# Kernel optimization log

Hardware: AMD Instinct MI355X
Metric: run time of the kernel (lower is better)

Reference implementation:

```python
import jax, jax.numpy as jnp
import numpy as np

B = 1024      # number of states
NP = 32       # SVGD particles per state
AD = 20       # act_dim
OD = 64       # obs_dim
H = 256       # critic hidden width
STEPS = 5     # num_svgd_steps
LR = 0.1      # svgd_lr (adaptive_lr disabled)
SP0 = 1.0     # svgd_sigma_p0
ALIM = 1.0    # act_limit


def _q(obs, X, w1, b1, w2, b2, w3, b3):
    h = jnp.concatenate([obs, X], axis=-1)
    h = jax.nn.relu(h @ w1 + b1)
    h = jax.nn.relu(h @ w2 + b2)
    return jnp.squeeze(h @ w3 + b3, -1)


def _rbf(X):
    # X: [B, NP, AD] -> K [B,NP,NP], diff [B,NP,NP,AD], gamma [B,1,1], K_grad [B,NP,NP,AD]
    diff = X[:, :, None, :] - X[:, None, :, :]
    dist_sq = jnp.sum(diff * diff, axis=-1)
    # adaptive bandwidth via median heuristic (adaptive_sig=True)
    med = jnp.median(dist_sq.reshape(dist_sq.shape[0], -1), axis=-1)
    sig_sq = med / (2.0 * jnp.log(NP + 1.0))
    gamma = (1.0 / (2.0 * sig_sq + 1e-8))[:, None, None]
    K = jnp.exp(-gamma * dist_sq)
    K_grad = -2.0 * gamma[..., None] * diff * K[..., None]  # d/dx_i K(x_i, x_j)
    return K, diff, gamma, K_grad


def setup_inputs():
    key = jax.random.key(0)
    ks = jax.random.split(key, 16)
    N = B * NP

    def lin(k, fi, fo):
        return (jax.random.normal(k, (fi, fo), jnp.float32) / np.sqrt(fi)).astype(jnp.float32)

    return {
        "obs": jax.random.normal(ks[0], (N, OD), jnp.float32),
        "a0": jax.random.normal(ks[1], (N, AD), jnp.float32) * np.sqrt(SP0),
        "q1_w1": lin(ks[2], OD + AD, H), "q1_b1": jnp.zeros((H,), jnp.float32),
        "q1_w2": lin(ks[3], H, H),       "q1_b2": jnp.zeros((H,), jnp.float32),
        "q1_w3": lin(ks[4], H, 1),       "q1_b3": jnp.zeros((1,), jnp.float32),
        "q2_w1": lin(ks[5], OD + AD, H), "q2_b1": jnp.zeros((H,), jnp.float32),
        "q2_w2": lin(ks[6], H, H),       "q2_b2": jnp.zeros((H,), jnp.float32),
        "q2_w3": lin(ks[7], H, 1),       "q2_b3": jnp.zeros((1,), jnp.float32),
    }


def reference(obs, a0, q1_w1, q1_b1, q1_w2, q1_b2, q1_w3, q1_b3,
              q2_w1, q2_b1, q2_w2, q2_b2, q2_w3, q2_b3):
    eye = jnp.eye(NP, dtype=a0.dtype)

    def q_min_sum(Xf):
        q1 = _q(obs, Xf, q1_w1, q1_b1, q1_w2, q1_b2, q1_w3, q1_b3)
        q2 = _q(obs, Xf, q2_w1, q2_b1, q2_w2, q2_b2, q2_w3, q2_b3)
        return jnp.sum(jnp.minimum(q1, q2))

    score_fn = jax.grad(q_min_sum)  # autograd score function

    def step(carry, _):
        a, logp = carry
        score = score_fn(a).reshape(-1, NP, AD)                 # [B,NP,AD]
        X = a.reshape(-1, NP, AD)
        K, diff, gamma, Kg = _rbf(X)
        phi = (jnp.einsum('bij,bjd->bid', K, score) + Kg.sum(axis=1)) / NP
        # log-prob correction terms (with_logprob=True)
        term1 = jnp.mean(jnp.sum(Kg * score[:, None, :, :], axis=-1), axis=2)     # [B,NP]
        inner = jnp.sum(jnp.transpose(Kg, (0, 2, 1, 3)) * diff, axis=-1) \
                - AD * (K - eye)
        term2 = -2.0 * gamma[:, :, 0] * jnp.mean(inner, axis=1)                   # [B,NP]
        logp = logp - LR * (term1 + term2)
        a = a + LR * phi.reshape(a.shape)                        # svgd_optim
        return (a, logp), None

    logp0 = jnp.zeros((B, NP), a0.dtype)
    (a, logp_svgd), _ = jax.lax.scan(step, (a0, logp0), None, length=STEPS)

    a_sq = ALIM * jnp.tanh(a)                                    # [B*NP, AD]
    logp_normal = (-AD * 0.5 * jnp.log(2.0 * jnp.pi * SP0)
                   - 0.5 / SP0 * jnp.sum(a0 * a0, axis=-1)).reshape(-1, NP)
    logp_tanh = -jnp.sum(2.0 * (jnp.log(2.0) - a - jax.nn.softplus(-2.0 * a)),
                         axis=-1).reshape(-1, NP)
    logp_a = jnp.mean(logp_normal + logp_svgd + logp_tanh, axis=-1)  # [B]
    return a_sq, logp_a
```

## Files before the change

### kernel.cpp

```cpp
#include <hip/hip_runtime.h>
#include <math.h>

#define NPART 32
#define ADIM  20
#define ODIM  64
#define HID   256
#define NSTEPS 5
#define LRC   0.1f
#define NBLK  512
#define LOG33 3.4965075614664802f
#define A0LD  104

typedef short bf8 __attribute__((ext_vector_type(8)));
typedef short s4b __attribute__((ext_vector_type(4)));
typedef float f4  __attribute__((ext_vector_type(4)));
typedef unsigned u4 __attribute__((ext_vector_type(4)));

#define OW1T(n) ((n)*24576)
#define OW2T(n) (49152 + (n)*65536)
#define OW2C(n) (180224 + (n)*65536)
#define OW1X(n) (311296 + (n)*8192)
#define WS_ELEMS 327680

__device__ __forceinline__ short f2bf(float x) {
    unsigned u = __float_as_uint(x);
    u += 0x7FFFu + ((u >> 16) & 1u);
    return (short)(u >> 16);
}
__device__ __forceinline__ short f2bfT(float x) {
    return (short)(__float_as_uint(x) >> 16);
}
__device__ __forceinline__ float bf2f(short s) {
    return __uint_as_float(((unsigned)(unsigned short)s) << 16);
}

#define MFMA(a,b,c) __builtin_amdgcn_mfma_f32_16x16x32_bf16((a),(b),(c),0,0,0)

__global__ void prep_weights(const float* __restrict__ w1a, const float* __restrict__ w2a,
                             const float* __restrict__ w3a, const float* __restrict__ w1b,
                             const float* __restrict__ w2b, const float* __restrict__ w3b,
                             unsigned short* __restrict__ ws)
{
    int idx = blockIdx.x * 256 + threadIdx.x;
    if (idx >= WS_ELEMS) return;
    float val;
    if (idx < 49152) {
        int net = idx / 24576, rem = idx % 24576;
        int n = rem / 96, k = rem % 96;
        const float* w1 = net ? w1b : w1a;
        val = (k < 84) ? w1[k*256 + n] : 0.f;
    } else if (idx < 180224) {
        int t2 = idx - 49152; int net = t2 / 65536, rem = t2 % 65536;
        int n = rem / 256, k = rem % 256;
        const float* w2 = net ? w2b : w2a;
        val = w2[k*256 + n];
    } else if (idx < 311296) {
        int t2 = idx - 180224; int net = t2 / 65536, rem = t2 % 65536;
        const float* w2 = net ? w2b : w2a;
        const float* w3 = net ? w3b : w3a;
        val = w2[rem] * w3[rem % 256];
    } else {
        int t2 = idx - 311296; int net = t2 / 8192, rem = t2 % 8192;
        int d = rem / 256, n = rem % 256;
        const float* w1 = net ? w1b : w1a;
        val = (d < 20) ? w1[(64 + d)*256 + n] : 0.f;
    }
    ws[idx] = (unsigned short)f2bf(val);
}

__global__ void __launch_bounds__(512, 4)
svgd_main(const float* __restrict__ obs,  const float* __restrict__ a0g,
          const float* __restrict__ b1a,  const float* __restrict__ b2a, const float* __restrict__ b3a,
          const float* __restrict__ b1b,  const float* __restrict__ b2b, const float* __restrict__ b3b,
          const float* __restrict__ w3af, const float* __restrict__ w3bf,
          const unsigned short* __restrict__ ws, float* __restrict__ out)
{
    __shared__ __align__(16) short A0s[64*A0LD];
    __shared__ __align__(16) short hbuf[64*264];
    __shared__ unsigned maskS[2][2][64][8];
    __shared__ float Xm[64*20];
    __shared__ float scoreS[64*21];
    __shared__ float qpart[2][8][64];
    __shared__ int   winsS[64];
    __shared__ float logps[64];
    __shared__ unsigned short lutI[496], lutJ[496];
    __shared__ float med2[4];
    __shared__ float qvS[64];
    __shared__ float normsS[64], rowKS[64];
    __shared__ __align__(16) float diagS[64];

    float* d2sF = (float*)hbuf;
    float* GSF  = ((float*)hbuf) + 2304;
    short* SBs  = hbuf + 9216;
    short* KbS  = hbuf + 9216;
    short* STbS = hbuf + 11776;
    short* XTbS = hbuf + 14336;

    const int t = threadIdx.x, b = blockIdx.x;
    const int lane = t & 63, wv = t >> 6;
    const int q = lane >> 4, mp = lane & 15;
    const int nb = wv * 32;

    for (int p = t; p < 64*ODIM; p += 512) {
        int i = p >> 6, d = p & 63;
        A0s[i*A0LD + d] = f2bfT(obs[(b*64 + i)*ODIM + d]);
    }
    for (int p = t; p < 64*ADIM; p += 512) {
        int i = p / 20, d = p - i*20;
        float v = a0g[(b*64 + i)*20 + d];
        Xm[p] = v;
        A0s[i*A0LD + 64 + d] = f2bfT(v);
    }
    for (int p = t; p < 64*12; p += 512) { int i = p/12, d = p - i*12; A0s[i*A0LD + 84 + d] = 0; }
    if (t < 496) {
        int i_ = 0, rem = t;
        while (rem >= 31 - i_) { rem -= 31 - i_; ++i_; }
        lutI[t] = (unsigned short)i_; lutJ[t] = (unsigned short)(i_ + 1 + rem);
    }
    if (t < 64) logps[t] = 0.f;
    __syncthreads();

    for (int step = 0; step < NSTEPS; ++step) {
        for (int net = 0; net < 2; ++net) {
            const unsigned short* w1t = ws + OW1T(net);
            const unsigned short* w2t = ws + OW2T(net);
            const float* b1p = net ? b1b : b1a;
            const float* b2p = net ? b2b : b2a;
            const float* w3p = net ? w3bf : w3af;

            f4 acc[4][2];
            #pragma unroll
            for (int h = 0; h < 4; ++h) { acc[h][0] = (f4){0,0,0,0}; acc[h][1] = (f4){0,0,0,0}; }
            {
                const unsigned short* bp0 = w1t + (size_t)(nb +      mp)*96 + q*8;
                const unsigned short* bp1 = w1t + (size_t)(nb + 16 + mp)*96 + q*8;
                bf8 bb0 = *(const bf8*)bp0, bb1 = *(const bf8*)bp1;
                #pragma unroll
                for (int k0 = 0; k0 < 96; k0 += 32) {
                    bf8 n0 = bb0, n1 = bb1;
                    if (k0 + 32 < 96) { n0 = *(const bf8*)(bp0 + k0 + 32); n1 = *(const bf8*)(bp1 + k0 + 32); }
                    #pragma unroll
                    for (int h = 0; h < 4; ++h) {
                        bf8 aa = *(const bf8*)&A0s[(h*16 + mp)*A0LD + k0 + q*8];
                        acc[h][0] = MFMA(aa, bb0, acc[h][0]);
                        acc[h][1] = MFMA(aa, bb1, acc[h][1]);
                    }
                    bb0 = n0; bb1 = n1;
                }
            }
            {
                float bias0 = b1p[nb + mp], bias1 = b1p[nb + 16 + mp];
                #pragma unroll
                for (int h = 0; h < 4; ++h) {
                    #pragma unroll
                    for (int r = 0; r < 4; ++r) {
                        float v0 = acc[h][0][r] + bias0;
                        float v1 = acc[h][1][r] + bias1;
                        bool p0 = v0 > 0.f, p1 = v1 > 0.f;
                        unsigned long long bal0 = __ballot(p0);
                        unsigned long long bal1 = __ballot(p1);
                        int row = h*16 + q*4 + r;
                        hbuf[row*264 + nb +      mp] = f2bfT(p0 ? v0 : 0.f);
                        hbuf[row*264 + nb + 16 + mp] = f2bfT(p1 ? v1 : 0.f);
                        if (mp == 0) {
                            unsigned w = (unsigned)((bal0 >> (q*16)) & 0xFFFFull)
                                       | (((unsigned)((bal1 >> (q*16)) & 0xFFFFull)) << 16);
                            maskS[net][0][row][wv] = w;
                        }
                    }
                }
            }
            __syncthreads();

            #pragma unroll
            for (int h = 0; h < 4; ++h) { acc[h][0] = (f4){0,0,0,0}; acc[h][1] = (f4){0,0,0,0}; }
            {
                const unsigned short* bp0 = w2t + (size_t)(nb +      mp)*256 + q*8;
                const unsigned short* bp1 = w2t + (size_t)(nb + 16 + mp)*256 + q*8;
                bf8 bb0 = *(const bf8*)bp0, bb1 = *(const bf8*)bp1;
                #pragma unroll
                for (int k0 = 0; k0 < 256; k0 += 32) {
                    bf8 n0 = bb0, n1 = bb1;
                    if (k0 + 32 < 256) { n0 = *(const bf8*)(bp0 + k0 + 32); n1 = *(const bf8*)(bp1 + k0 + 32); }
                    #pragma unroll
                    for (int h = 0; h < 4; ++h) {
                        bf8 aa = *(const bf8*)&hbuf[(h*16 + mp)*264 + k0 + q*8];
                        acc[h][0] = MFMA(aa, bb0, acc[h][0]);
                        acc[h][1] = MFMA(aa, bb1, acc[h][1]);
                    }
                    bb0 = n0; bb1 = n1;
                }
            }
            {
                float bias0 = b2p[nb + mp], bias1 = b2p[nb + 16 + mp];
                float w30   = w3p[nb + mp], w31   = w3p[nb + 16 + mp];
                float qp[4][4] = {{0,0,0,0},{0,0,0,0},{0,0,0,0},{0,0,0,0}};
                #pragma unroll
                for (int h = 0; h < 4; ++h) {
                    #pragma unroll
                    for (int r = 0; r < 4; ++r) {
                        float v0 = acc[h][0][r] + bias0;
                        float v1 = acc[h][1][r] + bias1;
                        bool p0 = v0 > 0.f, p1 = v1 > 0.f;
                        unsigned long long bal0 = __ballot(p0);
                        unsigned long long bal1 = __ballot(p1);
                        if (mp == 0) {
                            unsigned w = (unsigned)((bal0 >> (q*16)) & 0xFFFFull)
                                       | (((unsigned)((bal1 >> (q*16)) & 0xFFFFull)) << 16);
                            maskS[net][1][h*16 + q*4 + r][wv] = w;
                        }
                        qp[h][r] += (p0 ? v0 * w30 : 0.f) + (p1 ? v1 * w31 : 0.f);
                    }
                }
                #pragma unroll
                for (int d = 1; d < 16; d <<= 1)
                    #pragma unroll
                    for (int h = 0; h < 4; ++h)
                        #pragma unroll
                        for (int r = 0; r < 4; ++r)
                            qp[h][r] += __shfl_xor(qp[h][r], d, 64);
                if (mp == 0) {
                    #pragma unroll
                    for (int h = 0; h < 4; ++h)
                        #pragma unroll
                        for (int r = 0; r < 4; ++r)
                            qpart[net][wv][h*16 + q*4 + r] = qp[h][r];
                }
            }
            __syncthreads();
        }

        if (t < 64) {
            float q0 = b3a[0], q1 = b3b[0];
            #pragma unroll
            for (int w = 0; w < 8; ++w) { q0 += qpart[0][w][t]; q1 += qpart[1][w][t]; }
            winsS[t] = (q0 <= q1) ? 0 : 1;
        }
        __syncthreads();

        for (int net = 0; net < 2; ++net) {
            const unsigned short* w2c = ws + OW2C(net);

            f4 acc[4][2];
            #pragma unroll
            for (int h = 0; h < 4; ++h) { acc[h][0] = (f4){0,0,0,0}; acc[h][1] = (f4){0,0,0,0}; }
            int win[4];
            #pragma unroll
            for (int h = 0; h < 4; ++h) win[h] = (winsS[h*16 + mp] == net);
            {
                const unsigned short* bp0 = w2c + (size_t)(nb +      mp)*256 + q*8;
                const unsigned short* bp1 = w2c + (size_t)(nb + 16 + mp)*256 + q*8;
                bf8 bb0 = *(const bf8*)bp0, bb1 = *(const bf8*)bp1;
                #pragma unroll
                for (int k0 = 0; k0 < 256; k0 += 32) {
                    bf8 n0 = bb0, n1 = bb1;
                    if (k0 + 32 < 256) { n0 = *(const bf8*)(bp0 + k0 + 32); n1 = *(const bf8*)(bp1 + k0 + 32); }
                    #pragma unroll
                    for (int h = 0; h < 4; ++h) {
                        unsigned bits = win[h] ? ((maskS[net][1][h*16 + mp][k0 >> 5] >> (q*8)) & 0xFFu) : 0u;
                        u4 mw;
                        mw[0] = ((bits &   1u) ? 0x3F80u : 0u) | ((bits &   2u) ? 0x3F800000u : 0u);
                        mw[1] = ((bits &   4u) ? 0x3F80u : 0u) | ((bits &   8u) ? 0x3F800000u : 0u);
                        mw[2] = ((bits &  16u) ? 0x3F80u : 0u) | ((bits &  32u) ? 0x3F800000u : 0u);
                        mw[3] = ((bits &  64u) ? 0x3F80u : 0u) | ((bits & 128u) ? 0x3F800000u : 0u);
                        bf8 aa = __builtin_bit_cast(bf8, mw);
                        acc[h][0] = MFMA(aa, bb0, acc[h][0]);
                        acc[h][1] = MFMA(aa, bb1, acc[h][1]);
                    }
                    bb0 = n0; bb1 = n1;
                }
            }
            #pragma unroll
            for (int h = 0; h < 4; ++h) {
                #pragma unroll
                for (int s = 0; s < 2; ++s) {
                    int col = nb + s*16 + mp;
                    #pragma unroll
                    for (int r = 0; r < 4; ++r) {
                        int row = h*16 + q*4 + r;
                        bool on = (maskS[net][0][row][col >> 5] >> (col & 31)) & 1u;
                        hbuf[row*264 + col] = f2bfT(on ? acc[h][s][r] : 0.f);
                    }
                }
            }
            __syncthreads();
            {
                int mt = wv & 3, ch = wv >> 2;
                const unsigned short* w1x = ws + OW1X(net);
                const unsigned short* bp  = w1x + (size_t)(ch*16 + mp)*256 + q*8;
                f4 sa = (f4){0,0,0,0};
                bf8 bx = *(const bf8*)bp;
                #pragma unroll
                for (int k0 = 0; k0 < 256; k0 += 32) {
                    bf8 nx = bx;
                    if (k0 + 32 < 256) nx = *(const bf8*)(bp + k0 + 32);
                    bf8 aa = *(const bf8*)&hbuf[(mt*16 + mp)*264 + k0 + q*8];
                    sa = MFMA(aa, bx, sa);
                    bx = nx;
                }
                int colD = ch*16 + mp;
                if (colD < 20) {
                    #pragma unroll
                    for (int r = 0; r < 4; ++r) {
                        int row = mt*16 + q*4 + r;
                        if (net == 0) scoreS[row*21 + colD]  = sa[r];
                        else          scoreS[row*21 + colD] += sa[r];
                    }
                }
            }
            __syncthreads();
        }

        if (t < 64) {
            int st = t >> 5;
            float nrm = 0.f, dg = 0.f;
            #pragma unroll
            for (int d = 0; d < 20; ++d) {
                float xb = bf2f(A0s[t*A0LD + 64 + d]);
                nrm += xb * xb;
                float sv = scoreS[t*21 + d];
                float xv = Xm[t*20 + d];
                dg += xv * sv;
                short sb = f2bfT(sv);
                SBs[t*40 + d] = sb;
                STbS[st*1280 + d*40 + (t & 31)] = sb;
                XTbS[st*1280 + d*40 + (t & 31)] = f2bfT(xv);
            }
            #pragma unroll
            for (int d = 20; d < 32; ++d) SBs[t*40 + d] = 0;
            normsS[t] = nrm;
            diagS[t]  = dg;
        }
        __syncthreads();

        {
            int stw = wv >> 2, mt = (wv >> 1) & 1, nt = wv & 1;
            bf8 aa  = *(const bf8*)&A0s[(stw*32 + mt*16 + mp)*A0LD + 64 + q*8];
            bf8 bbx = *(const bf8*)&A0s[(stw*32 + nt*16 + mp)*A0LD + 64 + q*8];
            bf8 bbs = *(const bf8*)&SBs[(stw*32 + nt*16 + mp)*40 + q*8];
            f4 gx = MFMA(aa, bbx, ((f4){0,0,0,0}));
            f4 gs = MFMA(aa, bbs, ((f4){0,0,0,0}));
            int jl = nt*16 + mp;
            float nj = normsS[stw*32 + jl];
            #pragma unroll
            for (int r = 0; r < 4; ++r) {
                int il = mt*16 + q*4 + r;
                d2sF[stw*1152 + il*36 + jl] = normsS[stw*32 + il] + nj - 2.f*gx[r];
                GSF [stw*1152 + il*36 + jl] = gs[r];
            }
        }
        __syncthreads();

        if (wv < 2) {
            const float* base = d2sF + wv*1152;
            float v[8];
            #pragma unroll
            for (int i = 0; i < 8; ++i) {
                int e = lane*8 + i;
                v[i] = (e < 496) ? base[lutI[e]*36 + lutJ[e]] : 3.4e38f;
            }
            for (int k = 2; k <= 512; k <<= 1) {
                for (int jj = k >> 1; jj >= 8; jj >>= 1) {
                    int lm = jj >> 3;
                    #pragma unroll
                    for (int i = 0; i < 8; ++i) {
                        float w = __shfl_xor(v[i], lm, 64);
                        int p = lane*8 + i;
                        bool takeMin = (((p & k) == 0) == ((p & jj) == 0));
                        v[i] = takeMin ? fminf(v[i], w) : fmaxf(v[i], w);
                    }
                }
                int jj0 = (k >> 1) < 4 ? (k >> 1) : 4;
                for (int jj = jj0; jj >= 1; jj >>= 1) {
                    #pragma unroll
                    for (int i = 0; i < 8; ++i) {
                        if ((i & jj) == 0) {
                            int i2 = i | jj;
                            int p = lane*8 + i;
                            bool up = ((p & k) == 0);
                            float x = v[i], y = v[i2];
                            float mn = fminf(x, y), mx = fmaxf(x, y);
                            v[i] = up ? mn : mx; v[i2] = up ? mx : mn;
                        }
                    }
                }
            }
            if (lane == 29) med2[wv*2 + 0] = v[7];
            if (lane == 30) med2[wv*2 + 1] = v[0];
        }
        __syncthreads();

        {
            int i = t >> 3, stw = i >> 5, il = i & 31, j0 = (t & 7) * 4;
            float medv = 0.5f * (med2[stw*2] + med2[stw*2 + 1]);
            float gam  = 1.f / (2.f * (medv / (2.f * LOG33)) + 1e-8f);
            f4 d2 = *(const f4*)&d2sF[stw*1152 + il*36 + j0];
            f4 gs = *(const f4*)&GSF [stw*1152 + il*36 + j0];
            f4 dg = *(const f4*)&diagS[stw*32 + j0];
            float K0 = expf(-gam * d2[0]), K1 = expf(-gam * d2[1]);
            float K2 = expf(-gam * d2[2]), K3 = expf(-gam * d2[3]);
            s4b kb; kb[0] = f2bfT(K0); kb[1] = f2bfT(K1); kb[2] = f2bfT(K2); kb[3] = f2bfT(K3);
            *(s4b*)&KbS[stw*1280 + il*40 + j0] = kb;
            float sK   = K0 + K1 + K2 + K3;
            float sKGS = K0*gs[0] + K1*gs[1] + K2*gs[2] + K3*gs[3];
            float sKd2 = K0*d2[0] + K1*d2[1] + K2*d2[2] + K3*d2[3];
            float sKdg = K0*dg[0] + K1*dg[1] + K2*dg[2] + K3*dg[3];
            #pragma unroll
            for (int d = 1; d < 8; d <<= 1) {
                sK   += __shfl_xor(sK,   d, 64);
                sKGS += __shfl_xor(sKGS, d, 64);
                sKd2 += __shfl_xor(sKd2, d, 64);
                sKdg += __shfl_xor(sKdg, d, 64);
            }
            if ((t & 7) == 0) {
                rowKS[i] = sK;
                float sdots = sKGS - sKdg;
                float ssum  = -2.f*gam*sdots
                              - 2.f*gam*(2.f*gam*sKd2 - 20.f*(sK - 1.f));
                logps[i] -= LRC * (ssum * (1.f/32.f));
            }
        }
        __syncthreads();

        {
            int stw = wv >> 2, mt = (wv >> 1) & 1, nt = wv & 1;
            float medv = 0.5f * (med2[stw*2] + med2[stw*2 + 1]);
            float gam  = 1.f / (2.f * (medv / (2.f * LOG33)) + 1e-8f);
            bf8 aa  = *(const bf8*)&KbS [stw*1280 + (mt*16 + mp)*40 + q*8];
            bf8 b1v = *(const bf8*)&STbS[stw*1280 + (nt*16 + mp)*40 + q*8];
            bf8 b2v = *(const bf8*)&XTbS[stw*1280 + (nt*16 + mp)*40 + q*8];
            f4 ks = MFMA(aa, b1v, ((f4){0,0,0,0}));
            f4 kx = MFMA(aa, b2v, ((f4){0,0,0,0}));
            int dd = nt*16 + mp;
            if (dd < 20) {
                #pragma unroll
                for (int r = 0; r < 4; ++r) {
                    int gi = stw*32 + mt*16 + q*4 + r;
                    float xi  = Xm[gi*20 + dd];
                    float phi = (ks[r] + 2.f*gam*(xi*rowKS[gi] - kx[r])) * (1.f/32.f);
                    float nx  = xi + LRC * phi;
                    Xm[gi*20 + dd] = nx;
                    A0s[gi*A0LD + 64 + dd] = f2bfT(nx);
                }
            }
        }
        __syncthreads();
    }

    for (int p = t; p < 64*20; p += 512) {
        int i = p / 20, d = p - i*20;
        out[(b*64 + i)*20 + d] = tanhf(Xm[p]);
    }
    if (t < 64) {
        float lt = 0.f, s0 = 0.f;
        for (int d = 0; d < 20; ++d) {
            float a  = Xm[t*20 + d];
            float x  = -2.f * a;
            float sp = fmaxf(x, 0.f) + log1pf(expf(-fabsf(x)));
            lt -= 2.f * (0.69314718056f - a - sp);
            float v = a0g[(b*64 + t)*20 + d];
            s0 += v * v;
        }
        qvS[t] = -18.3787706641f - 0.5f*s0 + logps[t] + lt;
    }
    __syncthreads();
    if (t < 2) {
        float s = 0.f;
        for (int i = 0; i < 32; ++i) s += qvS[t*32 + i];
        out[1024*32*20 + b*2 + t] = s * (1.f/32.f);
    }
}

extern "C" void kernel_launch(void* const* d_in, const int* in_sizes, int n_in,
                              void* d_out, int out_size, void* d_ws, size_t ws_size,
                              hipStream_t stream) {
    unsigned short* ws = (unsigned short*)d_ws;
    prep_weights<<<(WS_ELEMS + 255)/256, 256, 0, stream>>>(
        (const float*)d_in[2],  (const float*)d_in[4],  (const float*)d_in[6],
        (const float*)d_in[8],  (const float*)d_in[10], (const float*)d_in[12], ws);
    svgd_main<<<NBLK, 512, 0, stream>>>(
        (const float*)d_in[0],  (const float*)d_in[1],
        (const float*)d_in[3],  (const float*)d_in[5],  (const float*)d_in[7],
        (const float*)d_in[9],  (const float*)d_in[11], (const float*)d_in[13],
        (const float*)d_in[6],  (const float*)d_in[12],
        ws, (float*)d_out);
}
```

Measured before the change: 488.5 us.

## Interleave the two critic networks' MLP stages to cut barriers and overlap work

Unrolls the per-network loops and interleaves their stages: net1's layer-1 GEMM is issued alongside net0's layer-2 GEMM, and net1's backward GEMM overlaps net0's input-gradient GEMM, so several block-wide barriers are removed. The min-Q winner selection is computed redundantly per lane from qpart, which removes the winsS shared array and one sync. The per-row norm/diag and final logp loops are spread across 8 threads each with shuffle reductions instead of running on 64 threads, and expf is replaced by __expf. In exchange, holding more live accumulators raises register pressure under launch_bounds(512,4), and __expf slightly reduces accuracy.

Result: slower. 1.082 ms (+121.4%).

```diff
diff --git a/kernel.cpp b/kernel.cpp
--- a/kernel.cpp
+++ b/kernel.cpp
@@ -81,7 +81,6 @@
     __shared__ float Xm[64*20];
     __shared__ float scoreS[64*21];
     __shared__ float qpart[2][8][64];
-    __shared__ int   winsS[64];
     __shared__ float logps[64];
     __shared__ unsigned short lutI[496], lutJ[496];
     __shared__ float med2[4];
@@ -121,62 +120,154 @@
     __syncthreads();
 
     for (int step = 0; step < NSTEPS; ++step) {
-        for (int net = 0; net < 2; ++net) {
-            const unsigned short* w1t = ws + OW1T(net);
-            const unsigned short* w2t = ws + OW2T(net);
-            const float* b1p = net ? b1b : b1a;
-            const float* b2p = net ? b2b : b2a;
-            const float* w3p = net ? w3bf : w3af;
-
+        {
             f4 acc[4][2];
             #pragma unroll
             for (int h = 0; h < 4; ++h) { acc[h][0] = (f4){0,0,0,0}; acc[h][1] = (f4){0,0,0,0}; }
             {
-                const unsigned short* bp0 = w1t + (size_t)(nb +      mp)*96 + q*8;
-                const unsigned short* bp1 = w1t + (size_t)(nb + 16 + mp)*96 + q*8;
-                bf8 bb0 = *(const bf8*)bp0, bb1 = *(const bf8*)bp1;
+                const unsigned short* bp0 = ws + OW1T(0) + (size_t)(nb +      mp)*96 + q*8;
+                const unsigned short* bp1 = ws + OW1T(0) + (size_t)(nb + 16 + mp)*96 + q*8;
                 #pragma unroll
                 for (int k0 = 0; k0 < 96; k0 += 32) {
-                    bf8 n0 = bb0, n1 = bb1;
-                    if (k0 + 32 < 96) { n0 = *(const bf8*)(bp0 + k0 + 32); n1 = *(const bf8*)(bp1 + k0 + 32); }
+                    bf8 b0 = *(const bf8*)(bp0 + k0);
+                    bf8 b1 = *(const bf8*)(bp1 + k0);
                     #pragma unroll
                     for (int h = 0; h < 4; ++h) {
                         bf8 aa = *(const bf8*)&A0s[(h*16 + mp)*A0LD + k0 + q*8];
-                        acc[h][0] = MFMA(aa, bb0, acc[h][0]);
-                        acc[h][1] = MFMA(aa, bb1, acc[h][1]);
-                    }
-                    bb0 = n0; bb1 = n1;
-                }
-            }
-            {
-                float bias0 = b1p[nb + mp], bias1 = b1p[nb + 16 + mp];
+                        acc[h][0] = MFMA(aa, b0, acc[h][0]);
+                        acc[h][1] = MFMA(aa, b1, acc[h][1]);
+                    }
+                }
+            }
+            float bias0 = b1a[nb + mp], bias1 = b1a[nb + 16 + mp];
+            #pragma unroll
+            for (int h = 0; h < 4; ++h) {
+                #pragma unroll
+                for (int r = 0; r < 4; ++r) {
+                    float v0 = acc[h][0][r] + bias0;
+                    float v1 = acc[h][1][r] + bias1;
+                    bool p0 = v0 > 0.f, p1 = v1 > 0.f;
+                    unsigned long long bal0 = __ballot(p0);
+                    unsigned long long bal1 = __ballot(p1);
+                    int row = h*16 + q*4 + r;
+                    hbuf[row*264 + nb +      mp] = f2bfT(p0 ? v0 : 0.f);
+                    hbuf[row*264 + nb + 16 + mp] = f2bfT(p1 ? v1 : 0.f);
+                    if (mp == 0) {
+                        unsigned w = (unsigned)((bal0 >> (q*16)) & 0xFFFFull)
+                                   | (((unsigned)((bal1 >> (q*16)) & 0xFFFFull)) << 16);
+                        maskS[0][0][row][wv] = w;
+                    }
+                }
+            }
+        }
+        __syncthreads();
+
+        f4 acc1[4][2];
+        f4 accL[4][2];
+        #pragma unroll
+        for (int h = 0; h < 4; ++h) {
+            acc1[h][0] = (f4){0,0,0,0}; acc1[h][1] = (f4){0,0,0,0};
+            accL[h][0] = (f4){0,0,0,0}; accL[h][1] = (f4){0,0,0,0};
+        }
+        {
+            const unsigned short* ap0 = ws + OW1T(1) + (size_t)(nb +      mp)*96 + q*8;
+            const unsigned short* ap1 = ws + OW1T(1) + (size_t)(nb + 16 + mp)*96 + q*8;
+            #pragma unroll
+            for (int k0 = 0; k0 < 96; k0 += 32) {
+                bf8 b0 = *(const bf8*)(ap0 + k0);
+                bf8 b1 = *(const bf8*)(ap1 + k0);
                 #pragma unroll
                 for (int h = 0; h < 4; ++h) {
-                    #pragma unroll
-                    for (int r = 0; r < 4; ++r) {
-                        float v0 = acc[h][0][r] + bias0;
-                        float v1 = acc[h][1][r] + bias1;
-                        bool p0 = v0 > 0.f, p1 = v1 > 0.f;
-                        unsigned long long bal0 = __ballot(p0);
-                        unsigned long long bal1 = __ballot(p1);
-                        int row = h*16 + q*4 + r;
-                        hbuf[row*264 + nb +      mp] = f2bfT(p0 ? v0 : 0.f);
-                        hbuf[row*264 + nb + 16 + mp] = f2bfT(p1 ? v1 : 0.f);
-                        if (mp == 0) {
-                            unsigned w = (unsigned)((bal0 >> (q*16)) & 0xFFFFull)
-                                       | (((unsigned)((bal1 >> (q*16)) & 0xFFFFull)) << 16);
-                            maskS[net][0][row][wv] = w;
-                        }
-                    }
-                }
-            }
-            __syncthreads();
-
+                    bf8 aa = *(const bf8*)&A0s[(h*16 + mp)*A0LD + k0 + q*8];
+                    acc1[h][0] = MFMA(aa, b0, acc1[h][0]);
+                    acc1[h][1] = MFMA(aa, b1, acc1[h][1]);
+                }
+            }
+        }
+        {
+            const unsigned short* bp0 = ws + OW2T(0) + (size_t)(nb +      mp)*256 + q*8;
+            const unsigned short* bp1 = ws + OW2T(0) + (size_t)(nb + 16 + mp)*256 + q*8;
+            #pragma unroll
+            for (int k0 = 0; k0 < 256; k0 += 32) {
+                bf8 b0 = *(const bf8*)(bp0 + k0);
+                bf8 b1 = *(const bf8*)(bp1 + k0);
+                #pragma unroll
+                for (int h = 0; h < 4; ++h) {
+                    bf8 aa = *(const bf8*)&hbuf[(h*16 + mp)*264 + k0 + q*8];
+                    accL[h][0] = MFMA(aa, b0, accL[h][0]);
+                    accL[h][1] = MFMA(aa, b1, accL[h][1]);
+                }
+            }
+        }
+        __syncthreads();
+
+        {
+            float bias0 = b1b[nb + mp], bias1 = b1b[nb + 16 + mp];
+            #pragma unroll
+            for (int h = 0; h < 4; ++h) {
+                #pragma unroll
+                for (int r = 0; r < 4; ++r) {
+                    float v0 = acc1[h][0][r] + bias0;
+                    float v1 = acc1[h][1][r] + bias1;
+                    bool p0 = v0 > 0.f, p1 = v1 > 0.f;
+                    unsigned long long bal0 = __ballot(p0);
+                    unsigned long long bal1 = __ballot(p1);
+                    int row = h*16 + q*4 + r;
+                    hbuf[row*264 + nb +      mp] = f2bfT(p0 ? v0 : 0.f);
+                    hbuf[row*264 + nb + 16 + mp] = f2bfT(p1 ? v1 : 0.f);
+                    if (mp == 0) {
+                        unsigned w = (unsigned)((bal0 >> (q*16)) & 0xFFFFull)
+                                   | (((unsigned)((bal1 >> (q*16)) & 0xFFFFull)) << 16);
+                        maskS[1][0][row][wv] = w;
+                    }
+                }
+            }
+        }
+        {
+            float bias0 = b2a[nb + mp], bias1 = b2a[nb + 16 + mp];
+            float w30   = w3af[nb + mp], w31   = w3af[nb + 16 + mp];
+            float qp[4][4] = {{0,0,0,0},{0,0,0,0},{0,0,0,0},{0,0,0,0}};
+            #pragma unroll
+            for (int h = 0; h < 4; ++h) {
+                #pragma unroll
+                for (int r = 0; r < 4; ++r) {
+                    float v0 = accL[h][0][r] + bias0;
+                    float v1 = accL[h][1][r] + bias1;
+                    bool p0 = v0 > 0.f, p1 = v1 > 0.f;
+                    unsigned long long bal0 = __ballot(p0);
+                    unsigned long long bal1 = __ballot(p1);
+                    if (mp == 0) {
+                        unsigned w = (unsigned)((bal0 >> (q*16)) & 0xFFFFull)
+                                   | (((unsigned)((bal1 >> (q*16)) & 0xFFFFull)) << 16);
+                        maskS[0][1][h*16 + q*4 + r][wv] = w;
+                    }
+                    qp[h][r] += (p0 ? v0 * w30 : 0.f) + (p1 ? v1 * w31 : 0.f);
+                }
+            }
+            #pragma unroll
+            for (int d = 1; d < 16; d <<= 1)
+                #pragma unroll
+                for (int h = 0; h < 4; ++h)
+                    #pragma unroll
+                    for (int r = 0; r < 4; ++r)
+                        qp[h][r] += __shfl_xor(qp[h][r], d, 64);
+            if (mp == 0) {
+                #pragma unroll
+                for (int h = 0; h < 4; ++h)
+                    #pragma unroll
+                    for (int r = 0; r < 4; ++r)
+                        qpart[0][wv][h*16 + q*4 + r] = qp[h][r];
+            }
+        }
+        __syncthreads();
+
+        {
+            f4 acc[4][2];
             #pragma unroll
             for (int h = 0; h < 4; ++h) { acc[h][0] = (f4){0,0,0,0}; acc[h][1] = (f4){0,0,0,0}; }
             {
-                const unsigned short* bp0 = w2t + (size_t)(nb +      mp)*256 + q*8;
-                const unsigned short* bp1 = w2t + (size_t)(nb + 16 + mp)*256 + q*8;
+                const unsigned short* bp0 = ws + OW2T(1) + (size_t)(nb +      mp)*256 + q*8;
+                const unsigned short* bp1 = ws + OW2T(1) + (size_t)(nb + 16 + mp)*256 + q*8;
                 bf8 bb0 = *(const bf8*)bp0, bb1 = *(const bf8*)bp1;
                 #pragma unroll
                 for (int k0 = 0; k0 < 256; k0 += 32) {
@@ -191,65 +282,62 @@
                     bb0 = n0; bb1 = n1;
                 }
             }
+            float bias0 = b2b[nb + mp], bias1 = b2b[nb + 16 + mp];
+            float w30   = w3bf[nb + mp], w31   = w3bf[nb + 16 + mp];
+            float qp[4][4] = {{0,0,0,0},{0,0,0,0},{0,0,0,0},{0,0,0,0}};
+            #pragma unroll
+            for (int h = 0; h < 4; ++h) {
+                #pragma unroll
+                for (int r = 0; r < 4; ++r) {
+                    float v0 = acc[h][0][r] + bias0;
+                    float v1 = acc[h][1][r] + bias1;
+                    bool p0 = v0 > 0.f, p1 = v1 > 0.f;
+                    unsigned long long bal0 = __ballot(p0);
+                    unsigned long long bal1 = __ballot(p1);
+                    if (mp == 0) {
+                        unsigned w = (unsigned)((bal0 >> (q*16)) & 0xFFFFull)
+                                   | (((unsigned)((bal1 >> (q*16)) & 0xFFFFull)) << 16);
+                        maskS[1][1][h*16 + q*4 + r][wv] = w;
+                    }
+                    qp[h][r] += (p0 ? v0 * w30 : 0.f) + (p1 ? v1 * w31 : 0.f);
+                }
+            }
+            #pragma unroll
+            for (int d = 1; d < 16; d <<= 1)
+                #pragma unroll
+                for (int h = 0; h < 4; ++h)
+                    #pragma unroll
+                    for (int r = 0; r < 4; ++r)
+                        qp[h][r] += __shfl_xor(qp[h][r], d, 64);
+            if (mp == 0) {
+                #pragma unroll
+                for (int h = 0; h < 4; ++h)
+                    #pragma unroll
+                    for (int r = 0; r < 4; ++r)
+                        qpart[1][wv][h*16 + q*4 + r] = qp[h][r];
+            }
+        }
+        __syncthreads();
+
+        int win1g[4];
+        {
+            float ba = b3a[0], bb_ = b3b[0];
+            int win0[4];
+            #pragma unroll
+            for (int h = 0; h < 4; ++h) {
+                int row = h*16 + mp;
+                float q0 = ba, q1 = bb_;
+                #pragma unroll
+                for (int w = 0; w < 8; ++w) { q0 += qpart[0][w][row]; q1 += qpart[1][w][row]; }
+                win0[h]  = (q0 <= q1) ? 1 : 0;
+                win1g[h] = 1 - win0[h];
+            }
+            f4 acc[4][2];
+            #pragma unroll
+            for (int h = 0; h < 4; ++h) { acc[h][0] = (f4){0,0,0,0}; acc[h][1] = (f4){0,0,0,0}; }
             {
-                float bias0 = b2p[nb + mp], bias1 = b2p[nb + 16 + mp];
-                float w30   = w3p[nb + mp], w31   = w3p[nb + 16 + mp];
-                float qp[4][4] = {{0,0,0,0},{0,0,0,0},{0,0,0,0},{0,0,0,0}};
-                #pragma unroll
-                for (int h = 0; h < 4; ++h) {
-                    #pragma unroll
-                    for (int r = 0; r < 4; ++r) {
-                        float v0 = acc[h][0][r] + bias0;
-                        float v1 = acc[h][1][r] + bias1;
-                        bool p0 = v0 > 0.f, p1 = v1 > 0.f;
-                        unsigned long long bal0 = __ballot(p0);
-                        unsigned long long bal1 = __ballot(p1);
-                        if (mp == 0) {
-                            unsigned w = (unsigned)((bal0 >> (q*16)) & 0xFFFFull)
-                                       | (((unsigned)((bal1 >> (q*16)) & 0xFFFFull)) << 16);
-                            maskS[net][1][h*16 + q*4 + r][wv] = w;
-                        }
-                        qp[h][r] += (p0 ? v0 * w30 : 0.f) + (p1 ? v1 * w31 : 0.f);
-                    }
-                }
-                #pragma unroll
-                for (int d = 1; d < 16; d <<= 1)
-                    #pragma unroll
-                    for (int h = 0; h < 4; ++h)
-                        #pragma unroll
-                        for (int r = 0; r < 4; ++r)
-                            qp[h][r] += __shfl_xor(qp[h][r], d, 64);
-                if (mp == 0) {
-                    #pragma unroll
-                    for (int h = 0; h < 4; ++h)
-                        #pragma unroll
-                        for (int r = 0; r < 4; ++r)
-                            qpart[net][wv][h*16 + q*4 + r] = qp[h][r];
-                }
-            }
-            __syncthreads();
-        }
-
-        if (t < 64) {
-            float q0 = b3a[0], q1 = b3b[0];
-            #pragma unroll
-            for (int w = 0; w < 8; ++w) { q0 += qpart[0][w][t]; q1 += qpart[1][w][t]; }
-            winsS[t] = (q0 <= q1) ? 0 : 1;
-        }
-        __syncthreads();
-
-        for (int net = 0; net < 2; ++net) {
-            const unsigned short* w2c = ws + OW2C(net);
-
-            f4 acc[4][2];
-            #pragma unroll
-            for (int h = 0; h < 4; ++h) { acc[h][0] = (f4){0,0,0,0}; acc[h][1] = (f4){0,0,0,0}; }
-            int win[4];
-            #pragma unroll
-            for (int h = 0; h < 4; ++h) win[h] = (winsS[h*16 + mp] == net);
-            {
-                const unsigned short* bp0 = w2c + (size_t)(nb +      mp)*256 + q*8;
-                const unsigned short* bp1 = w2c + (size_t)(nb + 16 + mp)*256 + q*8;
+                const unsigned short* bp0 = ws + OW2C(0) + (size_t)(nb +      mp)*256 + q*8;
+                const unsigned short* bp1 = ws + OW2C(0) + (size_t)(nb + 16 + mp)*256 + q*8;
                 bf8 bb0 = *(const bf8*)bp0, bb1 = *(const bf8*)bp1;
                 #pragma unroll
                 for (int k0 = 0; k0 < 256; k0 += 32) {
@@ -257,7 +345,7 @@
                     if (k0 + 32 < 256) { n0 = *(const bf8*)(bp0 + k0 + 32); n1 = *(const bf8*)(bp1 + k0 + 32); }
                     #pragma unroll
                     for (int h = 0; h < 4; ++h) {
-                        unsigned bits = win[h] ? ((maskS[net][1][h*16 + mp][k0 >> 5] >> (q*8)) & 0xFFu) : 0u;
+                        unsigned bits = win0[h] ? ((maskS[0][1][h*16 + mp][k0 >> 5] >> (q*8)) & 0xFFu) : 0u;
                         u4 mw;
                         mw[0] = ((bits &   1u) ? 0x3F80u : 0u) | ((bits &   2u) ? 0x3F800000u : 0u);
                         mw[1] = ((bits &   4u) ? 0x3F80u : 0u) | ((bits &   8u) ? 0x3F800000u : 0u);
@@ -278,58 +366,128 @@
                     #pragma unroll
                     for (int r = 0; r < 4; ++r) {
                         int row = h*16 + q*4 + r;
-                        bool on = (maskS[net][0][row][col >> 5] >> (col & 31)) & 1u;
+                        bool on = (maskS[0][0][row][col >> 5] >> (col & 31)) & 1u;
                         hbuf[row*264 + col] = f2bfT(on ? acc[h][s][r] : 0.f);
                     }
                 }
             }
-            __syncthreads();
-            {
-                int mt = wv & 3, ch = wv >> 2;
-                const unsigned short* w1x = ws + OW1X(net);
-                const unsigned short* bp  = w1x + (size_t)(ch*16 + mp)*256 + q*8;
-                f4 sa = (f4){0,0,0,0};
-                bf8 bx = *(const bf8*)bp;
-                #pragma unroll
-                for (int k0 = 0; k0 < 256; k0 += 32) {
-                    bf8 nx = bx;
-                    if (k0 + 32 < 256) nx = *(const bf8*)(bp + k0 + 32);
-                    bf8 aa = *(const bf8*)&hbuf[(mt*16 + mp)*264 + k0 + q*8];
-                    sa = MFMA(aa, bx, sa);
-                    bx = nx;
-                }
-                int colD = ch*16 + mp;
-                if (colD < 20) {
-                    #pragma unroll
-                    for (int r = 0; r < 4; ++r) {
-                        int row = mt*16 + q*4 + r;
-                        if (net == 0) scoreS[row*21 + colD]  = sa[r];
-                        else          scoreS[row*21 + colD] += sa[r];
-                    }
-                }
-            }
-            __syncthreads();
-        }
-
-        if (t < 64) {
-            int st = t >> 5;
+        }
+        __syncthreads();
+
+        f4 accB[4][2];
+        #pragma unroll
+        for (int h = 0; h < 4; ++h) { accB[h][0] = (f4){0,0,0,0}; accB[h][1] = (f4){0,0,0,0}; }
+        {
+            const unsigned short* bp0 = ws + OW2C(1) + (size_t)(nb +      mp)*256 + q*8;
+            const unsigned short* bp1 = ws + OW2C(1) + (size_t)(nb + 16 + mp)*256 + q*8;
+            bf8 bb0 = *(const bf8*)bp0, bb1 = *(const bf8*)bp1;
+            #pragma unroll
+            for (int k0 = 0; k0 < 256; k0 += 32) {
+                bf8 n0 = bb0, n1 = bb1;
+                if (k0 + 32 < 256) { n0 = *(const bf8*)(bp0 + k0 + 32); n1 = *(const bf8*)(bp1 + k0 + 32); }
+                #pragma unroll
+                for (int h = 0; h < 4; ++h) {
+                    unsigned bits = win1g[h] ? ((maskS[1][1][h*16 + mp][k0 >> 5] >> (q*8)) & 0xFFu) : 0u;
+                    u4 mw;
+                    mw[0] = ((bits &   1u) ? 0x3F80u : 0u) | ((bits &   2u) ? 0x3F800000u : 0u);
+                    mw[1] = ((bits &   4u) ? 0x3F80u : 0u) | ((bits &   8u) ? 0x3F800000u : 0u);
+                    mw[2] = ((bits &  16u) ? 0x3F80u : 0u) | ((bits &  32u) ? 0x3F800000u : 0u);
+                    mw[3] = ((bits &  64u) ? 0x3F80u : 0u) | ((bits & 128u) ? 0x3F800000u : 0u);
+                    bf8 aa = __builtin_bit_cast(bf8, mw);
+                    accB[h][0] = MFMA(aa, bb0, accB[h][0]);
+                    accB[h][1] = MFMA(aa, bb1, accB[h][1]);
+                }
+                bb0 = n0; bb1 = n1;
+            }
+        }
+        f4 sa0 = (f4){0,0,0,0};
+        {
+            int mt = wv & 3, ch = wv >> 2;
+            const unsigned short* bp = ws + OW1X(0) + (size_t)(ch*16 + mp)*256 + q*8;
+            bf8 bx = *(const bf8*)bp;
+            #pragma unroll
+            for (int k0 = 0; k0 < 256; k0 += 32) {
+                bf8 nx = bx;
+                if (k0 + 32 < 256) nx = *(const bf8*)(bp + k0 + 32);
+                bf8 aa = *(const bf8*)&hbuf[(mt*16 + mp)*264 + k0 + q*8];
+                sa0 = MFMA(aa, bx, sa0);
+                bx = nx;
+            }
+        }
+        __syncthreads();
+
+        #pragma unroll
+        for (int h = 0; h < 4; ++h) {
+            #pragma unroll
+            for (int s = 0; s < 2; ++s) {
+                int col = nb + s*16 + mp;
+                #pragma unroll
+                for (int r = 0; r < 4; ++r) {
+                    int row = h*16 + q*4 + r;
+                    bool on = (maskS[1][0][row][col >> 5] >> (col & 31)) & 1u;
+                    hbuf[row*264 + col] = f2bfT(on ? accB[h][s][r] : 0.f);
+                }
+            }
+        }
+        {
+            int mt = wv & 3, ch = wv >> 2;
+            int colD = ch*16 + mp;
+            if (colD < 20) {
+                #pragma unroll
+                for (int r = 0; r < 4; ++r)
+                    scoreS[(mt*16 + q*4 + r)*21 + colD] = sa0[r];
+            }
+        }
+        __syncthreads();
+
+        {
+            int mt = wv & 3, ch = wv >> 2;
+            const unsigned short* bp = ws + OW1X(1) + (size_t)(ch*16 + mp)*256 + q*8;
+            f4 sa = (f4){0,0,0,0};
+            bf8 bx = *(const bf8*)bp;
+            #pragma unroll
+            for (int k0 = 0; k0 < 256; k0 += 32) {
+                bf8 nx = bx;
+                if (k0 + 32 < 256) nx = *(const bf8*)(bp + k0 + 32);
+                bf8 aa = *(const bf8*)&hbuf[(mt*16 + mp)*264 + k0 + q*8];
+                sa = MFMA(aa, bx, sa);
+                bx = nx;
+            }
+            int colD = ch*16 + mp;
+            if (colD < 20) {
+                #pragma unroll
+                for (int r = 0; r < 4; ++r)
+                    scoreS[(mt*16 + q*4 + r)*21 + colD] += sa[r];
+            }
+        }
+        __syncthreads();
+
+        {
+            int i = t >> 3, j = t & 7, st = i >> 5;
             float nrm = 0.f, dg = 0.f;
             #pragma unroll
-            for (int d = 0; d < 20; ++d) {
-                float xb = bf2f(A0s[t*A0LD + 64 + d]);
-                nrm += xb * xb;
-                float sv = scoreS[t*21 + d];
-                float xv = Xm[t*20 + d];
-                dg += xv * sv;
-                short sb = f2bfT(sv);
-                SBs[t*40 + d] = sb;
-                STbS[st*1280 + d*40 + (t & 31)] = sb;
-                XTbS[st*1280 + d*40 + (t & 31)] = f2bfT(xv);
-            }
-            #pragma unroll
-            for (int d = 20; d < 32; ++d) SBs[t*40 + d] = 0;
-            normsS[t] = nrm;
-            diagS[t]  = dg;
+            for (int dd = 0; dd < 3; ++dd) {
+                int d = j + dd*8;
+                if (d < 20) {
+                    float xb = bf2f(A0s[i*A0LD + 64 + d]);
+                    nrm += xb * xb;
+                    float sv = scoreS[i*21 + d];
+                    float xv = Xm[i*20 + d];
+                    dg += xv * sv;
+                    short sb = f2bfT(sv);
+                    SBs[i*40 + d] = sb;
+                    STbS[st*1280 + d*40 + (i & 31)] = sb;
+                    XTbS[st*1280 + d*40 + (i & 31)] = f2bfT(xv);
+                }
+            }
+            SBs[i*40 + 20 + j] = 0;
+            if (j < 4) SBs[i*40 + 28 + j] = 0;
+            #pragma unroll
+            for (int d = 1; d < 8; d <<= 1) {
+                nrm += __shfl_xor(nrm, d, 64);
+                dg  += __shfl_xor(dg,  d, 64);
+            }
+            if (j == 0) { normsS[i] = nrm; diagS[i] = dg; }
         }
         __syncthreads();
 
@@ -397,8 +555,8 @@
             f4 d2 = *(const f4*)&d2sF[stw*1152 + il*36 + j0];
             f4 gs = *(const f4*)&GSF [stw*1152 + il*36 + j0];
             f4 dg = *(const f4*)&diagS[stw*32 + j0];
-            float K0 = expf(-gam * d2[0]), K1 = expf(-gam * d2[1]);
-            float K2 = expf(-gam * d2[2]), K3 = expf(-gam * d2[3]);
+            float K0 = __expf(-gam * d2[0]), K1 = __expf(-gam * d2[1]);
+            float K2 = __expf(-gam * d2[2]), K3 = __expf(-gam * d2[3]);
             s4b kb; kb[0] = f2bfT(K0); kb[1] = f2bfT(K1); kb[2] = f2bfT(K2); kb[3] = f2bfT(K3);
             *(s4b*)&KbS[stw*1280 + il*40 + j0] = kb;
             float sK   = K0 + K1 + K2 + K3;
@@ -451,17 +609,27 @@
         int i = p / 20, d = p - i*20;
         out[(b*64 + i)*20 + d] = tanhf(Xm[p]);
     }
-    if (t < 64) {
+    {
+        int i = t >> 3, j = t & 7;
         float lt = 0.f, s0 = 0.f;
-        for (int d = 0; d < 20; ++d) {
-            float a  = Xm[t*20 + d];
-            float x  = -2.f * a;
-            float sp = fmaxf(x, 0.f) + log1pf(expf(-fabsf(x)));
-            lt -= 2.f * (0.69314718056f - a - sp);
-            float v = a0g[(b*64 + t)*20 + d];
-            s0 += v * v;
-        }
-        qvS[t] = -18.3787706641f - 0.5f*s0 + logps[t] + lt;
+        #pragma unroll
+        for (int dd = 0; dd < 3; ++dd) {
+            int d = j + dd*8;
+            if (d < 20) {
+                float a  = Xm[i*20 + d];
+                float x  = -2.f * a;
+                float sp = fmaxf(x, 0.f) + log1pf(__expf(-fabsf(x)));
+                lt -= 2.f * (0.69314718056f - a - sp);
+                float v = a0g[(b*64 + i)*20 + d];
+                s0 += v * v;
+            }
+        }
+        #pragma unroll
+        for (int d = 1; d < 8; d <<= 1) {
+            lt += __shfl_xor(lt, d, 64);
+            s0 += __shfl_xor(s0, d, 64);
+        }
+        if (j == 0) qvS[i] = -18.3787706641f - 0.5f*s0 + logps[i] + lt;
     }
     __syncthreads();
     if (t < 2) {
```
